# Kernel optimization log

Hardware: AMD Instinct MI355X
Metric: run time of the kernel (lower is better)

The kernel has to match this reference:

```python
import jax, jax.numpy as jnp
import numpy as np

# Faithful JAX port of MLPVolatilityModelImproved.negative_log_likelihood
# (activation = relu, init_u2 = None path).
# NOTE: the original torch code builds T windows but u has T-1 elements, which
# would raise a shape error in the final sum; we use the standard GARCH
# alignment (n = T-1 windows, window t ends at u2_{t-1}) so everything lines up.


def setup_inputs() -> dict:
    key = jax.random.key(0)
    ks = jax.random.split(key, 8)
    T, k, q = 500_000, 32, 64
    r = 0.01 * jax.random.normal(ks[0], (T,), jnp.float32)          # returns
    volume = jax.random.uniform(ks[1], (T,), jnp.float32)            # volumes > 0
    a0 = jnp.zeros((), jnp.float32)
    a1 = jnp.zeros((), jnp.float32)
    raw_beta0 = jnp.asarray(-4.0, jnp.float32)
    raw_beta = -4.0 + 0.1 * jax.random.normal(ks[2], (k,), jnp.float32)
    raw_w0 = -8.0 + 0.1 * jax.random.normal(ks[3], (k,), jnp.float32)
    raw_w = -4.0 + 0.1 * jax.random.normal(ks[4], (k, q), jnp.float32)
    raw_gamma = -4.0 + 0.1 * jax.random.normal(ks[5], (k, q), jnp.float32)
    raw_rho = -4.0 + 0.1 * jax.random.normal(ks[6], (k,), jnp.float32)
    return {"r": r, "volume": volume, "a0": a0, "a1": a1,
            "raw_beta0": raw_beta0, "raw_beta": raw_beta, "raw_w0": raw_w0,
            "raw_w": raw_w, "raw_gamma": raw_gamma, "raw_rho": raw_rho}


def reference(r, volume, a0, a1, raw_beta0, raw_beta, raw_w0, raw_w, raw_gamma, raw_rho):
    q = raw_w.shape[1]
    sp = jax.nn.softplus
    beta0, beta, w0, w, gamma, rho = sp(raw_beta0), sp(raw_beta), sp(raw_w0), sp(raw_w), sp(raw_gamma), sp(raw_rho)

    u = r[1:] - a0 - a1 * r[:-1]          # [T-1] residuals
    u2 = u * u
    n = u2.shape[0]                        # T-1 steps

    # torch.var is unbiased (ddof=1); .detach() -> stop_gradient
    var_u2 = jax.lax.stop_gradient(jnp.var(u2, ddof=1))
    init_u2 = var_u2 * jnp.ones((q,), u2.dtype)
    u2_full = jnp.concatenate([init_u2, u2])                              # [q+T-1]
    vol_full = jnp.concatenate([jnp.broadcast_to(volume[0], (q,)), volume[:-1]])

    # unfold(0, q, 1).flip(1): row t, col j = x[t + q - 1 - j]
    idx = jnp.arange(n)[:, None] + (q - 1) - jnp.arange(q)[None, :]       # [n, q]
    u2_w = u2_full[idx]
    vol_w = vol_full[idx]

    # [n, k] static pre-activations
    static_input = w0[None, :] + u2_w @ w.T + vol_w @ gamma.T

    sigma2_init = var_u2 + 1e-6

    def step(sigma2_prev, s_in):
        h = jax.nn.relu(s_in + rho * sigma2_prev)      # [k]
        val = beta0 + jnp.dot(h, beta) + 1e-8
        return val, val

    _, sigmas2 = jax.lax.scan(step, sigma2_init, static_input)            # [n]

    nll = (0.5 * n * jnp.log(jnp.asarray(2.0 * np.pi, sigmas2.dtype))
           + 0.5 * jnp.sum(jnp.log(sigmas2))
           + 0.5 * jnp.sum(u2 / sigmas2))
    return nll
```

## Files before the change

### kernel.cpp

```cpp
#include <hip/hip_runtime.h>
#include <math.h>

#define KCH 32
#define Q 64

#define TB 256
#define TILE (TB + Q)
#define USTR 352

#define LCH 28
#define WSC 12
#define QPB 64

typedef __attribute__((ext_vector_type(8))) short short8;
typedef __attribute__((ext_vector_type(4))) float float4v;

__device__ __forceinline__ float sp_softplus(float x) {
    return (x > 15.f) ? x : log1pf(expf(x));
}

__device__ __forceinline__ unsigned int f2bf(float f) {
    union { float f; unsigned int u; } v; v.f = f;
    unsigned int u = v.u;
    return (u + 0x7FFFu + ((u >> 16) & 1u)) >> 16;
}

__device__ __forceinline__ float bflo(unsigned int w) {
    return __int_as_float((int)(w << 16));
}
__device__ __forceinline__ float bfhi(unsigned int w) {
    return __int_as_float((int)(w & 0xFFFF0000u));
}

__device__ __forceinline__ float quad_sum4(float v) {
    int vi = __float_as_int(v);
    int p1 = __builtin_amdgcn_update_dpp(0, vi, 0xB1, 0xF, 0xF, true);
    v += __int_as_float(p1);
    vi = __float_as_int(v);
    int p2 = __builtin_amdgcn_update_dpp(0, vi, 0x4E, 0xF, 0xF, true);
    v += __int_as_float(p2);
    return v;
}

#define WOFF_BF16W 4352
#define WOFF_U2    6656

extern "C" __global__ void k12_stats(const float* __restrict__ r,
                                     const float* __restrict__ a0p,
                                     const float* __restrict__ a1p,
                                     const float* __restrict__ rb0,
                                     const float* __restrict__ rb,
                                     const float* __restrict__ rw0,
                                     const float* __restrict__ rw,
                                     const float* __restrict__ rg,
                                     const float* __restrict__ rr,
                                     float* __restrict__ wsf,
                                     int n, int nblocks) {
    const float a0 = a0p[0], a1 = a1p[0];
    float s1 = 0.f, s2 = 0.f;
    for (int t = blockIdx.x * blockDim.x + threadIdx.x; t < n;
         t += gridDim.x * blockDim.x) {
        float u = r[t + 1] - a0 - a1 * r[t];
        float u2 = u * u;
        s1 += u2;
        s2 += u2 * u2;
    }
#pragma unroll
    for (int off = 32; off > 0; off >>= 1) {
        s1 += __shfl_down(s1, off);
        s2 += __shfl_down(s2, off);
    }
    __shared__ float b1[4], b2[4];
    __shared__ int lastflag;
    int wid = threadIdx.x >> 6;
    if ((threadIdx.x & 63) == 0) { b1[wid] = s1; b2[wid] = s2; }
    __syncthreads();
    if (threadIdx.x == 0) {
        float t1 = b1[0] + b1[1] + b1[2] + b1[3];
        float t2 = b2[0] + b2[1] + b2[2] + b2[3];
        atomicAdd(&wsf[0], t1);
        atomicAdd(&wsf[1], t2);
        __threadfence();
        int old = atomicAdd((int*)(wsf + 7), 1);
        lastflag = (old == nblocks - 1) ? 1 : 0;
    }
    __syncthreads();
    if (!lastflag) return;

    const int tid = threadIdx.x;
    if (tid == 0) {
        float t1 = atomicAdd(&wsf[0], 0.f);
        float t2 = atomicAdd(&wsf[1], 0.f);
        float nf = (float)n;
        float mean = t1 / nf;
        float var = fmaxf((t2 - nf * mean * mean) / (nf - 1.f), 0.f);
        wsf[2] = var;
        wsf[3] = var + 1e-6f;
        wsf[6] = sp_softplus(rb0[0]);
    }
    if (tid < KCH) {
        wsf[8 + tid]  = sp_softplus(rb[tid]);
        wsf[40 + tid] = sp_softplus(rr[tid]);
        wsf[72 + tid] = sp_softplus(rw0[tid]);
    }
    unsigned short* Wb = (unsigned short*)(wsf + WOFF_BF16W);
    for (int idx = tid; idx < 2 * KCH * Q; idx += blockDim.x) {
        int k = idx >> 5;
        int i = idx & 31;
        float raw = (k < Q) ? rw[i * Q + (Q - 1 - k)]
                            : rg[i * Q + (Q - 1 - (k - Q))];
        Wb[idx] = (unsigned short)f2bf(sp_softplus(raw));
    }
}

extern "C" __global__ void __launch_bounds__(256)
k3c_mfma(const float* __restrict__ r, const float* __restrict__ vol,
         const float* __restrict__ a0p, const float* __restrict__ a1p,
         const float* __restrict__ wsf,
         unsigned int* __restrict__ s32, float* __restrict__ u2_out, int n) {
    __shared__ unsigned short UV[4 * USTR];
    unsigned short* Ue = UV;
    unsigned short* Uo = UV + USTR;
    unsigned short* Ve = UV + 2 * USTR;
    unsigned short* Vo = UV + 3 * USTR;

    const int t0 = blockIdx.x * TB;
    const float a0 = a0p[0], a1 = a1p[0];
    const float var = wsf[2];

    for (int x = threadIdx.x; x < TILE; x += 256) {
        int f = t0 + x;
        float uval, vval;
        if (f < Q) {
            uval = var;
            vval = vol[0];
        } else {
            int t = f - Q;
            uval = 0.f; vval = 0.f;
            if (t < n) {
                float u = r[t + 1] - a0 - a1 * r[t];
                uval = u * u;
                vval = vol[t];
                u2_out[t] = uval;
            }
        }
        unsigned short ub = (unsigned short)f2bf(uval);
        unsigned short vb = (unsigned short)f2bf(vval);
        Ue[x] = ub; Ve[x] = vb;
        if (x > 0) { Uo[x - 1] = ub; Vo[x - 1] = vb; }
    }
    __syncthreads();

    const int tid = threadIdx.x;
    const int lane = tid & 63;
    const int ln = lane & 15;
    const int q4 = (lane >> 4) & 3;
    const int q8 = q4 * 8;
    const int wv = tid >> 6;

    const unsigned short* Wb = (const unsigned short*)(wsf + WOFF_BF16W);
    short8 bf[4][2];
#pragma unroll
    for (int c = 0; c < 4; c++)
#pragma unroll
        for (int h = 0; h < 2; h++)
#pragma unroll
            for (int j = 0; j < 8; j++)
                bf[c][h][j] = (short)Wb[(c * 32 + q8 + j) * 32 + 2 * ln + h];
    const float w00 = wsf[72 + 2 * ln];
    const float w01 = wsf[72 + 2 * ln + 1];

    const unsigned int* pUe = (const unsigned int*)Ue;
    const unsigned int* pUo = (const unsigned int*)Uo;
    const unsigned int* pVe = (const unsigned int*)Ve;
    const unsigned int* pVo = (const unsigned int*)Vo;

#pragma unroll
    for (int wt = 0; wt < 4; wt++) {
        const int st = wv * 64 + wt * 16;
        float4v acc0 = {0.f, 0.f, 0.f, 0.f};
        float4v acc1 = {0.f, 0.f, 0.f, 0.f};
#pragma unroll
        for (int c = 0; c < 4; c++) {
            int e0 = st + ln + (c & 1) * 32 + q8;
            const unsigned int* pe = (c < 2) ? pUe : pVe;
            const unsigned int* po = (c < 2) ? pUo : pVo;
            const unsigned int* p = (e0 & 1) ? po : pe;
            int hx = e0 >> 1;
            union { unsigned int w[4]; short8 s; } A;
            A.w[0] = p[hx];
            A.w[1] = p[hx + 1];
            A.w[2] = p[hx + 2];
            A.w[3] = p[hx + 3];
            acc0 = __builtin_amdgcn_mfma_f32_16x16x32_bf16(A.s, bf[c][0], acc0, 0, 0, 0);
            acc1 = __builtin_amdgcn_mfma_f32_16x16x32_bf16(A.s, bf[c][1], acc1, 0, 0, 0);
        }
        const int rowb = t0 + st + q4 * 4;
#pragma unroll
        for (int rg_ = 0; rg_ < 4; rg_++) {
            int t = rowb + rg_;
            if (t < n) {
                unsigned int lo = f2bf(acc0[rg_] + w00);
                unsigned int hi = f2bf(acc1[rg_] + w01);
                s32[(size_t)t * 16 + ln] = lo | (hi << 16);
            }
        }
    }
}

extern "C" __global__ void __launch_bounds__(256, 4)
k3s_scan(const unsigned short* __restrict__ s, const float* __restrict__ u2a,
         float* __restrict__ wsf, float* __restrict__ out,
         int n, int C, int nwaves) {
    const int tid = threadIdx.x;
    const int quad = tid >> 2;
    const int laneq = tid & 3;
    const int chunk = blockIdx.x * QPB + quad;

    float rho_c[8], beta_c[8];
#pragma unroll
    for (int e = 0; e < 8; e++) {
        rho_c[e]  = wsf[40 + laneq * 8 + e];
        beta_c[e] = wsf[8 + laneq * 8 + e];
    }
    const float bconst = wsf[6] + 1e-8f;
    float sig = wsf[3];
    float sumlog = 0.f, sumratio = 0.f;

    int base = 0, warm = 0, send = 0;
    if (chunk < C) {
        const int cstart = chunk * LCH;
        warm = (chunk == 0) ? 0 : WSC;
        base = cstart - warm;
        send = warm + min(LCH, n - cstart);
    }
    const int send4 = (send + 3) & ~3;
    const char* sb = (const char*)s + laneq * 16;

    uint4 bq[4];
    float bu[4];
#pragma unroll
    for (int d = 0; d < 4; d++) {
        int tt = (d < send) ? (base + d) : 0;
        bq[d] = *reinterpret_cast<const uint4*>(sb + (size_t)tt * 64);
        bu[d] = u2a[tt];
    }

#define SCAN_STEP(d)                                                          \
    {                                                                         \
        const int s2 = s0 + (d);                                              \
        uint4 Wd = bq[d]; float uu = bu[d];                                   \
        int tn = base + s2 + 4; tn = (tn < n) ? tn : (n - 1);                 \
        bq[d] = *reinterpret_cast<const uint4*>(sb + (size_t)tn * 64);        \
        bu[d] = u2a[tn];                                                      \
        float h0 = fmaxf(fmaf(rho_c[0], sig, bflo(Wd.x)), 0.f);               \
        float h1 = fmaxf(fmaf(rho_c[1], sig, bfhi(Wd.x)), 0.f);               \
        float h2 = fmaxf(fmaf(rho_c[2], sig, bflo(Wd.y)), 0.f);               \
        float h3 = fmaxf(fmaf(rho_c[3], sig, bfhi(Wd.y)), 0.f);               \
        float h4 = fmaxf(fmaf(rho_c[4], sig, bflo(Wd.z)), 0.f);               \
        float h5 = fmaxf(fmaf(rho_c[5], sig, bfhi(Wd.z)), 0.f);               \
        float h6 = fmaxf(fmaf(rho_c[6], sig, bflo(Wd.w)), 0.f);               \
        float h7 = fmaxf(fmaf(rho_c[7], sig, bfhi(Wd.w)), 0.f);               \
        float p0 = beta_c[0] * h0;                                            \
        float p1 = beta_c[1] * h1;                                            \
        p0 = fmaf(beta_c[2], h2, p0);                                         \
        p1 = fmaf(beta_c[3], h3, p1);                                         \
        p0 = fmaf(beta_c[4], h4, p0);                                         \
        p1 = fmaf(beta_c[5], h5, p1);                                         \
        p0 = fmaf(beta_c[6], h6, p0);                                         \
        p1 = fmaf(beta_c[7], h7, p1);                                         \
        float dsum = quad_sum4(p0 + p1);                                      \
        sig = bconst + dsum;                                                  \
        float logv = __logf(sig);                                             \
        float rat = uu * __builtin_amdgcn_rcpf(sig);                          \
        bool live = (s2 >= warm) && (s2 < send);                              \
        sumlog += live ? logv : 0.f;                                          \
        sumratio += live ? rat : 0.f;                                         \
    }

    for (int s0 = 0; s0 < send4; s0 += 4) {
        SCAN_STEP(0)
        SCAN_STEP(1)
        SCAN_STEP(2)
        SCAN_STEP(3)
    }
#undef SCAN_STEP

    if (laneq != 0) { sumlog = 0.f; sumratio = 0.f; }
#pragma unroll
    for (int off = 32; off > 0; off >>= 1) {
        sumlog   += __shfl_down(sumlog, off);
        sumratio += __shfl_down(sumratio, off);
    }
    if ((tid & 63) == 0) {
        atomicAdd(&wsf[4], sumlog);
        atomicAdd(&wsf[5], sumratio);
        __threadfence();
        int old = atomicAdd((int*)(wsf + 104), 1);
        if (old == nwaves - 1) {
            float sl = atomicAdd(&wsf[4], 0.f);
            float sr = atomicAdd(&wsf[5], 0.f);
            double cst = 0.5 * (double)n * 1.8378770664093454;
            out[0] = (float)(cst + 0.5 * (double)sl + 0.5 * (double)sr);
        }
    }
}

extern "C" void kernel_launch(void* const* d_in, const int* in_sizes, int n_in,
                              void* d_out, int out_size, void* d_ws, size_t ws_size,
                              hipStream_t stream) {
    const float* r   = (const float*)d_in[0];
    const float* vol = (const float*)d_in[1];
    const float* a0  = (const float*)d_in[2];
    const float* a1  = (const float*)d_in[3];
    const float* rb0 = (const float*)d_in[4];
    const float* rb  = (const float*)d_in[5];
    const float* rw0 = (const float*)d_in[6];
    const float* rw  = (const float*)d_in[7];
    const float* rg  = (const float*)d_in[8];
    const float* rr  = (const float*)d_in[9];
    float* wsf = (float*)d_ws;
    float* out = (float*)d_out;
    const int T = in_sizes[0];
    const int n = T - 1;

    const size_t u2_off = WOFF_U2;
    const size_t s_off  = u2_off + (size_t)((n + 255) & ~255);
    float* u2a = wsf + u2_off;
    unsigned int* s32 = (unsigned int*)(wsf + s_off);

    hipMemsetAsync(wsf, 0, 512, stream);
    hipLaunchKernelGGL(k12_stats, dim3(256), dim3(256), 0, stream,
                       r, a0, a1, rb0, rb, rw0, rw, rg, rr, wsf, n, 256);
    const int nb_conv = (n + TB - 1) / TB;
    hipLaunchKernelGGL(k3c_mfma, dim3(nb_conv), dim3(256), 0, stream,
                       r, vol, a0, a1, wsf, s32, u2a, n);
    const int C = (n + LCH - 1) / LCH;
    const int nb_scan = (C + QPB - 1) / QPB;
    hipLaunchKernelGGL(k3s_scan, dim3(nb_scan), dim3(256), 0, stream,
                       (const unsigned short*)s32, u2a, wsf, out,
                       n, C, nb_scan * 4);
}
```

Before: 159.8 us.

## Shrink scan chunks to 8 steps with 8-step warmup and full unroll

Cuts each chunk's live length from 28 to 8 steps and its warmup from 12 to 8, so the fixed-length serial recurrence per thread is 16 steps instead of about 40. This shortens the latency-bound critical path at the cost of more total redundant warmup work, and raises the occupancy hint from 4 to 6 blocks. The u2 values are now loaded as two float4 vectors up front, and the step loop is fully unrolled with compile-time prefetch offsets instead of clamped runtime ones. The unclamped tail reads and the shorter warmup risk out-of-bounds reads and reduced accuracy of the warm-started sigma.

```diff
diff --git a/kernel.cpp b/kernel.cpp
--- a/kernel.cpp
+++ b/kernel.cpp
@@ -8,8 +8,9 @@
 #define TILE (TB + Q)
 #define USTR 352
 
-#define LCH 28
-#define WSC 12
+#define LCH 8
+#define WSC 8
+#define NST 16
 #define QPB 64
 
 typedef __attribute__((ext_vector_type(8))) short short8;
@@ -208,7 +209,7 @@
     }
 }
 
-extern "C" __global__ void __launch_bounds__(256, 4)
+extern "C" __global__ void __launch_bounds__(256, 6)
 k3s_scan(const unsigned short* __restrict__ s, const float* __restrict__ u2a,
          float* __restrict__ wsf, float* __restrict__ out,
          int n, int C, int nwaves) {
@@ -225,66 +226,55 @@
     }
     const float bconst = wsf[6] + 1e-8f;
     float sig = wsf[3];
-    float sumlog = 0.f, sumratio = 0.f;
-
-    int base = 0, warm = 0, send = 0;
+
+    int base = 0, warm = WSC, lcnt = 0;
     if (chunk < C) {
         const int cstart = chunk * LCH;
-        warm = (chunk == 0) ? 0 : WSC;
-        base = cstart - warm;
-        send = warm + min(LCH, n - cstart);
-    }
-    const int send4 = (send + 3) & ~3;
-    const char* sb = (const char*)s + laneq * 16;
+        if (chunk == 0) { warm = 0; base = 0; }
+        else            { base = cstart - WSC; }
+        lcnt = min(LCH, n - cstart);
+    }
+    const char* sb = (const char*)s + (size_t)base * 64 + laneq * 16;
+
+    float4 ua0 = *reinterpret_cast<const float4*>(u2a + base + warm);
+    float4 ua1 = *reinterpret_cast<const float4*>(u2a + base + warm + 4);
+    float uu[8] = {ua0.x, ua0.y, ua0.z, ua0.w, ua1.x, ua1.y, ua1.z, ua1.w};
 
     uint4 bq[4];
-    float bu[4];
-#pragma unroll
-    for (int d = 0; d < 4; d++) {
-        int tt = (d < send) ? (base + d) : 0;
-        bq[d] = *reinterpret_cast<const uint4*>(sb + (size_t)tt * 64);
-        bu[d] = u2a[tt];
-    }
-
-#define SCAN_STEP(d)                                                          \
-    {                                                                         \
-        const int s2 = s0 + (d);                                              \
-        uint4 Wd = bq[d]; float uu = bu[d];                                   \
-        int tn = base + s2 + 4; tn = (tn < n) ? tn : (n - 1);                 \
-        bq[d] = *reinterpret_cast<const uint4*>(sb + (size_t)tn * 64);        \
-        bu[d] = u2a[tn];                                                      \
-        float h0 = fmaxf(fmaf(rho_c[0], sig, bflo(Wd.x)), 0.f);               \
-        float h1 = fmaxf(fmaf(rho_c[1], sig, bfhi(Wd.x)), 0.f);               \
-        float h2 = fmaxf(fmaf(rho_c[2], sig, bflo(Wd.y)), 0.f);               \
-        float h3 = fmaxf(fmaf(rho_c[3], sig, bfhi(Wd.y)), 0.f);               \
-        float h4 = fmaxf(fmaf(rho_c[4], sig, bflo(Wd.z)), 0.f);               \
-        float h5 = fmaxf(fmaf(rho_c[5], sig, bfhi(Wd.z)), 0.f);               \
-        float h6 = fmaxf(fmaf(rho_c[6], sig, bflo(Wd.w)), 0.f);               \
-        float h7 = fmaxf(fmaf(rho_c[7], sig, bfhi(Wd.w)), 0.f);               \
-        float p0 = beta_c[0] * h0;                                            \
-        float p1 = beta_c[1] * h1;                                            \
-        p0 = fmaf(beta_c[2], h2, p0);                                         \
-        p1 = fmaf(beta_c[3], h3, p1);                                         \
-        p0 = fmaf(beta_c[4], h4, p0);                                         \
-        p1 = fmaf(beta_c[5], h5, p1);                                         \
-        p0 = fmaf(beta_c[6], h6, p0);                                         \
-        p1 = fmaf(beta_c[7], h7, p1);                                         \
-        float dsum = quad_sum4(p0 + p1);                                      \
-        sig = bconst + dsum;                                                  \
-        float logv = __logf(sig);                                             \
-        float rat = uu * __builtin_amdgcn_rcpf(sig);                          \
-        bool live = (s2 >= warm) && (s2 < send);                              \
-        sumlog += live ? logv : 0.f;                                          \
-        sumratio += live ? rat : 0.f;                                         \
-    }
-
-    for (int s0 = 0; s0 < send4; s0 += 4) {
-        SCAN_STEP(0)
-        SCAN_STEP(1)
-        SCAN_STEP(2)
-        SCAN_STEP(3)
-    }
-#undef SCAN_STEP
+#pragma unroll
+    for (int d = 0; d < 4; d++)
+        bq[d] = *reinterpret_cast<const uint4*>(sb + d * 64);
+
+    float sumlog = 0.f, sumratio = 0.f;
+#pragma unroll
+    for (int s2 = 0; s2 < NST; s2++) {
+        uint4 Wd = bq[s2 & 3];
+        if (s2 < NST - 4)
+            bq[s2 & 3] = *reinterpret_cast<const uint4*>(sb + (s2 + 4) * 64);
+        float h0 = fmaxf(fmaf(rho_c[0], sig, bflo(Wd.x)), 0.f);
+        float h1 = fmaxf(fmaf(rho_c[1], sig, bfhi(Wd.x)), 0.f);
+        float h2 = fmaxf(fmaf(rho_c[2], sig, bflo(Wd.y)), 0.f);
+        float h3 = fmaxf(fmaf(rho_c[3], sig, bfhi(Wd.y)), 0.f);
+        float h4 = fmaxf(fmaf(rho_c[4], sig, bflo(Wd.z)), 0.f);
+        float h5 = fmaxf(fmaf(rho_c[5], sig, bfhi(Wd.z)), 0.f);
+        float h6 = fmaxf(fmaf(rho_c[6], sig, bflo(Wd.w)), 0.f);
+        float h7 = fmaxf(fmaf(rho_c[7], sig, bfhi(Wd.w)), 0.f);
+        float p0 = beta_c[0] * h0;
+        float p1 = beta_c[1] * h1;
+        p0 = fmaf(beta_c[2], h2, p0);
+        p1 = fmaf(beta_c[3], h3, p1);
+        p0 = fmaf(beta_c[4], h4, p0);
+        p1 = fmaf(beta_c[5], h5, p1);
+        p0 = fmaf(beta_c[6], h6, p0);
+        p1 = fmaf(beta_c[7], h7, p1);
+        float dsum = quad_sum4(p0 + p1);
+        sig = bconst + dsum;
+        float uuv = (warm == 0) ? ((s2 < 8) ? uu[s2] : 0.f)
+                                : ((s2 >= 8) ? uu[s2 - 8] : 0.f);
+        bool live = (s2 >= warm) && ((s2 - warm) < lcnt);
+        sumlog   += live ? __logf(sig) : 0.f;
+        sumratio += live ? uuv * __builtin_amdgcn_rcpf(sig) : 0.f;
+    }
 
     if (laneq != 0) { sumlog = 0.f; sumratio = 0.f; }
 #pragma unroll
```

New measurement: 237.7 us. 1.49x slower.
